# Optimization experiments

Measured on AMD Instinct MI355X. Metric: run time of the kernel, lower is better.

Reference implementation:

```python
import jax, jax.numpy as jnp
import numpy as np
from jax import lax

ALPHA = 2.0   # snntorch surrogate.atan(alpha=2.0)
THR = 1.0     # snntorch Leaky default threshold
NUM_STEPS = 8

@jax.custom_vjp
def spike(x):
    # Heaviside forward, ATan surrogate backward (matches snntorch surrogate.atan)
    return (x > 0).astype(x.dtype)

def _spk_fwd(x):
    return (x > 0).astype(x.dtype), x

def _spk_bwd(x, g):
    return (g * (ALPHA / 2.0) / (1.0 + (jnp.pi / 2.0 * ALPHA * x) ** 2),)

spike.defvjp(_spk_fwd, _spk_bwd)


def setup_inputs() -> dict:
    key = jax.random.key(0)
    ks = jax.random.split(key, 7)
    B, D, H, A = 16384, 512, 2048, 8
    H2 = H // 2
    s1 = 1.0 / np.sqrt(D)
    s2 = 1.0 / np.sqrt(H)
    s3 = 1.0 / np.sqrt(H2)
    return {
        "x": jax.random.normal(ks[0], (B, D), jnp.float32),
        "W1": jax.random.uniform(ks[1], (H, D), jnp.float32, -s1, s1),
        "b1": jax.random.uniform(ks[2], (H,), jnp.float32, -s1, s1),
        "W2": jax.random.uniform(ks[3], (H2, H), jnp.float32, -s2, s2),
        "b2": jax.random.uniform(ks[4], (H2,), jnp.float32, -s2, s2),
        "Wo": jax.random.uniform(ks[5], (A, H2), jnp.float32, -s3, s3),
        "bo": jax.random.uniform(ks[6], (A,), jnp.float32, -s3, s3),
        "beta1": jnp.float32(0.9),
        "beta2": jnp.float32(0.85),
        "beta_out": jnp.float32(0.95),
    }


def reference(x, W1, b1, W2, b2, Wo, bo, beta1, beta2, beta_out):
    B = x.shape[0]
    H, H2, A = W1.shape[0], W2.shape[0], Wo.shape[0]
    # snntorch clamps learnable beta into [0, 1] inside the state function
    be1 = jnp.clip(beta1, 0.0, 1.0)
    be2 = jnp.clip(beta2, 0.0, 1.0)
    beo = jnp.clip(beta_out, 0.0, 1.0)

    cur1 = x @ W1.T + b1  # fc1(x) is identical every step; hoist out of the loop

    mem1 = jnp.zeros((B, H), x.dtype)
    mem2 = jnp.zeros((B, H2), x.dtype)
    mem_out = jnp.zeros((B, A), x.dtype)
    max_mem = jnp.full((B, A), -1e9, x.dtype)

    def step(carry, _):
        mem1, mem2, mem_out, max_mem = carry
        # lif1: subtract-reset Leaky; reset uses detached spike of previous mem
        reset1 = lax.stop_gradient(spike(mem1 - THR))
        mem1 = be1 * mem1 + cur1 - reset1 * THR
        spk1 = spike(mem1 - THR)
        # lif2
        reset2 = lax.stop_gradient(spike(mem2 - THR))
        mem2 = be2 * mem2 + (spk1 @ W2.T + b2) - reset2 * THR
        spk2 = spike(mem2 - THR)
        # li_out: reset_mechanism='none' -> pure leaky integrator
        mem_out = beo * mem_out + (spk2 @ Wo.T + bo)
        max_mem = jnp.maximum(max_mem, mem_out)
        return (mem1, mem2, mem_out, max_mem), None

    (mem1, mem2, mem_out, max_mem), _ = lax.scan(
        step, (mem1, mem2, mem_out, max_mem), None, length=NUM_STEPS
    )
    return max_mem
```

## Files before the change

kernel.cpp:

```cpp
#include <hip/hip_runtime.h>
#include <stdint.h>


typedef __bf16 bf16;
typedef __attribute__((ext_vector_type(8))) __bf16 bf16x8;
typedef __attribute__((ext_vector_type(4))) float f32x4;

#define CAP1 2097152
#define CAP2 2097152
#define MARGIN 2e-3f
#define MARGIN2 5e-4f

__device__ __forceinline__ void gl16(const void* g, void* l) {
  __builtin_amdgcn_global_load_lds(
      (const __attribute__((address_space(1))) uint32_t*)g,
      (__attribute__((address_space(3))) uint32_t*)l, 16, 0, 0);
}

__device__ __forceinline__ float clampf(float v) {
  return fminf(fmaxf(v, 0.f), 1.f);
}

__device__ __forceinline__ uint32_t expand2(uint32_t b) {
  return ((b & 1u) ? 0x3F80u : 0u) | ((b & 2u) ? 0x3F800000u : 0u);
}


__global__ void split_x_kernel(const float* __restrict__ x, bf16* __restrict__ Ax) {
  int i = blockIdx.x * 256 + threadIdx.x;
  int b = i >> 9, d = i & 511;
  float v = x[i];
  bf16 hi = (bf16)v;
  bf16 lo = (bf16)(v - (float)hi);
  size_t base = (size_t)b * 1024;
  Ax[base + d] = hi;
  Ax[base + 512 + d] = lo;
}

__global__ void split_w1_kernel(const float* __restrict__ W1, bf16* __restrict__ B0,
                                bf16* __restrict__ B1) {
  int i = blockIdx.x * 256 + threadIdx.x;
  int r = i >> 9, d = i & 511;
  float v = W1[i];
  bf16 hi = (bf16)v;
  bf16 lo = (bf16)(v - (float)hi);
  size_t base = (size_t)r * 1024;
  B0[base + d] = hi;  B0[base + 512 + d] = lo;
  B1[base + d] = lo;  B1[base + 512 + d] = hi;
}

__global__ void split_w2_kernel(const float* __restrict__ W2, bf16* __restrict__ Wh,
                                bf16* __restrict__ Wl) {
  int i = blockIdx.x * 256 + threadIdx.x;
  float v = W2[i];
  bf16 hi = (bf16)v;
  Wh[i] = hi;
  Wl[i] = (bf16)(v - (float)hi);
}


#define SA_OFF  0
#define SB0_OFF 16384
#define SB1_OFF 32768

__global__ __launch_bounds__(256, 2) void gemm1_lif1_kernel(
    const bf16* __restrict__ A, const bf16* __restrict__ B0,
    const bf16* __restrict__ B1, const float* __restrict__ bias,
    const float* __restrict__ beta1p,
    uint32_t* __restrict__ spkbits1, uint2* __restrict__ flag1,
    uint32_t* __restrict__ cnt1)
{
  __shared__ __align__(16) uint8_t lds[49152];
  const int tid = threadIdx.x;
  const int lane = tid & 63;
  const int wave = tid >> 6;
  const int wm = (wave >> 1) * 64, wn = (wave & 1) * 64;
  const size_t brow = (size_t)blockIdx.x * 128;
  const size_t bcol = (size_t)blockIdx.y * 128;
  const int K = 1024;
  const float be = clampf(beta1p[0]);

  const bf16* gA  = A  + brow * K;
  const bf16* gB0 = B0 + bcol * K;
  const bf16* gB1 = B1 + bcol * K;

  f32x4 acc[4][4] = {};

  for (int kk = 0; kk < K; kk += 64) {
#pragma unroll
    for (int q = 0; q < 4; ++q) {
      const int flat = q * 256 + tid;
      const int row = flat >> 3;
      const int s   = flat & 7;
      const int c8  = (s ^ (row & 7)) * 8;
      gl16(gA  + (size_t)row * K + kk + c8, lds + SA_OFF  + flat * 16);
      gl16(gB0 + (size_t)row * K + kk + c8, lds + SB0_OFF + flat * 16);
      gl16(gB1 + (size_t)row * K + kk + c8, lds + SB1_OFF + flat * 16);
    }
    asm volatile("s_waitcnt vmcnt(0)" ::: "memory");
    __syncthreads();
#pragma unroll
    for (int ks = 0; ks < 2; ++ks) {
      bf16x8 af[4], b0f[4], b1f[4];
#pragma unroll
      for (int i = 0; i < 4; ++i) {
        const int ra = wm + i * 16 + (lane & 15);
        const int sa = ((ks * 4 + (lane >> 4)) ^ (ra & 7)) * 16;
        af[i]  = *(const bf16x8*)(lds + SA_OFF  + ra * 128 + sa);
        const int rb = wn + i * 16 + (lane & 15);
        const int sb = ((ks * 4 + (lane >> 4)) ^ (rb & 7)) * 16;
        b0f[i] = *(const bf16x8*)(lds + SB0_OFF + rb * 128 + sb);
        b1f[i] = *(const bf16x8*)(lds + SB1_OFF + rb * 128 + sb);
      }
#pragma unroll
      for (int m = 0; m < 4; ++m)
#pragma unroll
        for (int n = 0; n < 4; ++n) {
          acc[m][n] = __builtin_amdgcn_mfma_f32_16x16x32_bf16(af[m], b0f[n], acc[m][n], 0, 0, 0);
          acc[m][n] = __builtin_amdgcn_mfma_f32_16x16x32_bf16(af[m], b1f[n], acc[m][n], 0, 0, 0);
        }
    }
    __syncthreads();
  }

  uint32_t* lcnt  = (uint32_t*)lds;
  uint32_t* lbase = (uint32_t*)(lds + 4);
  uint2*    llist = (uint2*)(lds + 16);
  const uint32_t CAPL = 3000;
  if (tid == 0) *lcnt = 0;
  __syncthreads();

  const int rg = lane >> 4;
  const bool writer = (lane & 15) == 0;
  uint16_t* sp16 = (uint16_t*)spkbits1;

#pragma unroll
  for (int m = 0; m < 4; ++m)
#pragma unroll
    for (int n = 0; n < 4; ++n) {
      const int chb = (int)(bcol) + wn + n * 16;
      const int w32 = chb >> 5, half = (chb >> 4) & 1;
      const float bv = bias[chb + (lane & 15)];
#pragma unroll
      for (int j = 0; j < 4; ++j) {
        const float c = acc[m][n][j] + bv;
        float mem = 0.f; uint32_t hist = 0; bool nearThr = false;
#pragma unroll
        for (int t = 0; t < 8; ++t) {
          float rst = (mem > 1.f) ? 1.f : 0.f;
          mem = be * mem + c - rst;
          uint32_t bit = (mem > 1.f) ? 1u : 0u;
          hist |= bit << t;
          nearThr |= (fabsf(mem - 1.f) < MARGIN);
        }
#pragma unroll
        for (int t = 0; t < 8; ++t) {
          unsigned long long bal = __ballot((hist >> t) & 1u);
          if (writer) {
            uint32_t row = (uint32_t)(brow + wm + m * 16 + rg * 4 + j);
            size_t idx = ((size_t)(t * 64 + w32) * 16384 + row) * 2 + half;
            sp16[idx] = (uint16_t)(bal >> (rg * 16));
          }
        }
        if (nearThr) {
          const uint32_t h = (uint32_t)(chb + (lane & 15));
          const uint32_t b = (uint32_t)(brow + wm + m * 16 + rg * 4 + j);
          uint2 en; en.x = (h << 14) | b; en.y = hist;
          uint32_t pos = atomicAdd(lcnt, 1u);
          if (pos < CAPL) llist[pos] = en;
          else { uint32_t g = atomicAdd(cnt1, 1u); if (g < CAP1) flag1[g] = en; }
        }
      }
    }

  __syncthreads();
  uint32_t ln = *lcnt; if (ln > CAPL) ln = CAPL;
  if (tid == 0) *lbase = atomicAdd(cnt1, ln);
  __syncthreads();
  const uint32_t gb = *lbase;
  for (uint32_t i = tid; i < ln; i += 256) {
    uint32_t g = gb + i;
    if (g < CAP1) flag1[g] = llist[i];
  }
}


__global__ __launch_bounds__(256) void repair1_kernel(
    const float* __restrict__ x, const float* __restrict__ W1,
    const float* __restrict__ b1, const float* __restrict__ beta1p,
    const uint2* __restrict__ flag1, const uint32_t* __restrict__ cnt1,
    uint32_t* __restrict__ spkbits1)
{
  uint32_t n = cnt1[0]; if (n > CAP1) n = CAP1;
  const float be = clampf(beta1p[0]);
  for (uint32_t i = blockIdx.x * 256 + threadIdx.x; i < n; i += gridDim.x * 256) {
    uint2 e = flag1[i];
    int h = e.x >> 14, b = e.x & 16383;
    const float* xr = x + (size_t)b * 512;
    const float* wr = W1 + (size_t)h * 512;
    float s = 0.f;
    for (int d = 0; d < 512; ++d) s = fmaf(xr[d], wr[d], s);
    s = __fadd_rn(s, b1[h]);
    float m = 0.f; uint32_t eb = 0;
#pragma unroll
    for (int t = 0; t < 8; ++t) {
      float rst = (__fsub_rn(m, 1.f) > 0.f) ? 1.f : 0.f;
      m = __fsub_rn(__fadd_rn(__fmul_rn(be, m), s), rst);
      if (__fsub_rn(m, 1.f) > 0.f) eb |= 1u << t;
    }
    uint32_t diff = eb ^ (e.y & 0xFFu);
    if (diff) {
#pragma unroll
      for (int t = 0; t < 8; ++t)
        if ((diff >> t) & 1u)
          atomicXor(&spkbits1[((size_t)t * 64 + (h >> 5)) * 16384 + b], 1u << (h & 31));
    }
  }
}


#define BOFF(d) ((d) * 16384)

__global__ __launch_bounds__(256, 3) void step2_kernel(
    const uint32_t* __restrict__ spkbits1,
    const bf16* __restrict__ W2h, const bf16* __restrict__ W2l,
    const float* __restrict__ b2, const float* __restrict__ beta2p,
    uint32_t* __restrict__ spkbits2, uint32_t* __restrict__ flag2,
    uint32_t* __restrict__ cnt2)
{
  __shared__ __align__(16) uint8_t lds[32768];
  const int K = 2048;
  const int tid = threadIdx.x;
  const int lane = tid & 63;
  const int wave = tid >> 6;
  const int wm = (wave >> 1) * 64, wn = (wave & 1) * 64;
  const size_t brow = (size_t)blockIdx.x * 128;
  const size_t bcol = (size_t)blockIdx.y * 128;
  const float be2 = clampf(beta2p[0]);

  const bf16* gB0 = W2h + bcol * K;
  const bf16* gB1 = W2l + bcol * K;

  float b2c[4];
#pragma unroll
  for (int n = 0; n < 4; ++n) b2c[n] = b2[bcol + wn + n * 16 + (lane & 15)];

  const int rg = lane >> 4;
  const int lnlo = lane & 15;
  const int sh8 = rg * 8;
  const bool writer = lnlo == 0;
  uint16_t* sp16 = (uint16_t*)spkbits2;

  f32x4 acc[4][4] = {};
  unsigned long long flg = 0;

#define STAGE_B(D, KC)                                                        \
  {                                                                           \
    _Pragma("unroll")                                                         \
    for (int q = 0; q < 2; ++q) {                                             \
      const int flat = q * 256 + tid;                                         \
      const int row = flat >> 2;                                              \
      const int s = flat & 3;                                                 \
      const int c8 = (s ^ ((row >> 1) & 3)) * 8;                              \
      gl16(gB0 + (size_t)row * K + (KC) * 32 + c8, lds + BOFF(D) + flat * 16);\
      gl16(gB1 + (size_t)row * K + (KC) * 32 + c8,                            \
           lds + BOFF(D) + 8192 + flat * 16);                                 \
    }                                                                         \
  }

#define LOAD_A(AW, TT, KC)                                                    \
  {                                                                           \
    const uint32_t* pA =                                                      \
        spkbits1 + ((size_t)((TT) * 64 + (KC))) * 16384 + brow;               \
    _Pragma("unroll")                                                         \
    for (int i = 0; i < 4; ++i) AW[i] = pA[wm + i * 16 + lnlo];               \
  }

#define CHUNK(CUR, NXT, TT_N, KC_N, D)                                        \
  {                                                                           \
    LOAD_A(NXT, TT_N, KC_N);                                                  \
    STAGE_B(D ^ 1, KC_N);                                                     \
    bf16x8 af[4];                                                             \
    _Pragma("unroll")                                                         \
    for (int i = 0; i < 4; ++i) {                                             \
      uint32_t byte = (CUR[i] >> sh8) & 0xFFu;                                \
      uint4 u;                                                                \
      u.x = expand2(byte);                                                    \
      u.y = expand2(byte >> 2);                                               \
      u.z = expand2(byte >> 4);                                               \
      u.w = expand2(byte >> 6);                                               \
      af[i] = *(bf16x8*)&u;                                                   \
    }                                                                         \
    asm volatile("s_waitcnt vmcnt(8)" ::: "memory");                          \
    __builtin_amdgcn_s_barrier();                                             \
    bf16x8 b0f[4], b1f[4];                                                    \
    _Pragma("unroll")                                                         \
    for (int i = 0; i < 4; ++i) {                                             \
      const int rb = wn + i * 16 + lnlo;                                      \
      const int sb = (rg ^ ((rb >> 1) & 3)) * 16;                             \
      b0f[i] = *(const bf16x8*)(lds + BOFF(D) + rb * 64 + sb);                \
      b1f[i] = *(const bf16x8*)(lds + BOFF(D) + 8192 + rb * 64 + sb);         \
    }                                                                         \
    _Pragma("unroll")                                                         \
    for (int m = 0; m < 4; ++m)                                               \
      _Pragma("unroll")                                                       \
      for (int n = 0; n < 4; ++n) {                                           \
        acc[m][n] = __builtin_amdgcn_mfma_f32_16x16x32_bf16(                  \
            af[m], b0f[n], acc[m][n], 0, 0, 0);                               \
        acc[m][n] = __builtin_amdgcn_mfma_f32_16x16x32_bf16(                  \
            af[m], b1f[n], acc[m][n], 0, 0, 0);                               \
      }                                                                       \
    __builtin_amdgcn_s_barrier();                                             \
  }

  uint32_t awA[4], awB[4];

  LOAD_A(awA, 0, 0);
  STAGE_B(0, 0);

  for (int t = 0; t < 8; ++t) {
#pragma unroll
    for (int m = 0; m < 4; ++m)
#pragma unroll
      for (int n = 0; n < 4; ++n)
#pragma unroll
        for (int j = 0; j < 4; ++j) {
          float v = acc[m][n][j];
          float rst = (v > 1.f) ? 1.f : 0.f;
          acc[m][n][j] = be2 * v + (b2c[n] - rst);
        }

#pragma unroll 1
    for (int kc2 = 0; kc2 < 32; ++kc2) {
      CHUNK(awA, awB, t, 2 * kc2 + 1, 0)
      {
        const int kcn = (2 * kc2 + 2) & 63;
        const int tn = (kc2 == 31 && t < 7) ? t + 1 : t;
        CHUNK(awB, awA, tn, kcn, 1)
      }
    }

#pragma unroll
    for (int m = 0; m < 4; ++m)
#pragma unroll
      for (int n = 0; n < 4; ++n) {
        const int chb = (int)(bcol) + wn + n * 16;
        const int w32 = chb >> 5, half = (chb >> 4) & 1;
#pragma unroll
        for (int j = 0; j < 4; ++j) {
          float v = acc[m][n][j];
          if (fabsf(v - 1.f) < MARGIN2) flg |= 1ull << (m * 16 + n * 4 + j);
          unsigned long long bal = __ballot(v > 1.f);
          if (writer) {
            uint32_t row = (uint32_t)(brow + wm + m * 16 + rg * 4 + j);
            size_t idx = ((size_t)(t * 32 + w32) * 16384 + row) * 2 + half;
            sp16[idx] = (uint16_t)(bal >> (rg * 16));
          }
        }
      }
  }

  asm volatile("s_waitcnt vmcnt(0)" ::: "memory");
  __syncthreads();
  uint32_t* lcnt  = (uint32_t*)lds;
  uint32_t* lbase = (uint32_t*)(lds + 4);
  uint32_t* llist = (uint32_t*)(lds + 16);
  const uint32_t CAPL = 6000;
  if (tid == 0) *lcnt = 0;
  __syncthreads();

  if (flg) {
#pragma unroll
    for (int m = 0; m < 4; ++m)
#pragma unroll
      for (int n = 0; n < 4; ++n)
#pragma unroll
        for (int j = 0; j < 4; ++j)
          if ((flg >> (m * 16 + n * 4 + j)) & 1ull) {
            const int row = wm + m * 16 + rg * 4 + j;
            const int col = wn + n * 16 + lnlo;
            uint32_t en = (uint32_t)(((brow + row) << 10) | (bcol + col));
            uint32_t pos = atomicAdd(lcnt, 1u);
            if (pos < CAPL) llist[pos] = en;
            else { uint32_t g = atomicAdd(cnt2, 1u); if (g < CAP2) flag2[g] = en; }
          }
  }

  __syncthreads();
  uint32_t ln = *lcnt; if (ln > CAPL) ln = CAPL;
  if (tid == 0) *lbase = atomicAdd(cnt2, ln);
  __syncthreads();
  const uint32_t gb = *lbase;
  for (uint32_t i = tid; i < ln; i += 256) {
    uint32_t g = gb + i;
    if (g < CAP2) flag2[g] = llist[i];
  }
#undef STAGE_B
#undef LOAD_A
#undef CHUNK
}


__global__ __launch_bounds__(256) void repair2_kernel(
    const uint32_t* __restrict__ spkbits1, const float* __restrict__ W2,
    const float* __restrict__ b2, const float* __restrict__ beta2p,
    const uint32_t* __restrict__ flag2, const uint32_t* __restrict__ cnt2,
    uint32_t* __restrict__ spkbits2)
{
  uint32_t n = cnt2[0]; if (n > CAP2) n = CAP2;
  const float be = clampf(beta2p[0]);
  for (uint32_t i = blockIdx.x * 256 + threadIdx.x; i < n; i += gridDim.x * 256) {
    uint32_t e = flag2[i];
    int b = e >> 10, h2 = e & 1023;
    const float* wr = W2 + (size_t)h2 * 2048;
    const float bias = b2[h2];
    float s[8] = {0, 0, 0, 0, 0, 0, 0, 0};
    for (int w = 0; w < 64; ++w) {
      uint32_t bt[8];
#pragma unroll
      for (int t = 0; t < 8; ++t)
        bt[t] = spkbits1[((size_t)t * 64 + w) * 16384 + b];
#pragma unroll 8
      for (int k = 0; k < 32; ++k) {
        const float wv = wr[w * 32 + k];
#pragma unroll
        for (int t = 0; t < 8; ++t) {
          float addend = ((bt[t] >> k) & 1u) ? wv : 0.0f;
          s[t] = __fadd_rn(s[t], addend);
        }
      }
    }
    float m = 0.f;
#pragma unroll
    for (int t = 0; t < 8; ++t) {
      float st = __fadd_rn(s[t], bias);
      float rst = (__fsub_rn(m, 1.f) > 0.f) ? 1.f : 0.f;
      m = __fsub_rn(__fadd_rn(__fmul_rn(be, m), st), rst);
      uint32_t exact = (__fsub_rn(m, 1.f) > 0.f) ? 1u : 0u;
      uint32_t* wp = &spkbits2[((size_t)t * 32 + (h2 >> 5)) * 16384 + b];
      uint32_t stored = (*wp >> (h2 & 31)) & 1u;
      if (stored != exact) atomicXor(wp, 1u << (h2 & 31));
    }
  }
}


__global__ __launch_bounds__(256) void out_kernel(
    const uint32_t* __restrict__ spkbits2, const float* __restrict__ Wo,
    const float* __restrict__ bo, const float* __restrict__ betaop,
    float* __restrict__ out)
{
  const int wave = threadIdx.x >> 6, lane = threadIdx.x & 63;
  const int b = blockIdx.x * 4 + wave;
  const float beo = clampf(betaop[0]);
  const int a = lane & 7;
  const int slice = lane >> 3;

  float s[8] = {0, 0, 0, 0, 0, 0, 0, 0};
#pragma unroll
  for (int q = 0; q < 4; ++q) {
    const int wrd = slice * 4 + q;
    uint32_t wt[8];
#pragma unroll
    for (int t = 0; t < 8; ++t)
      wt[t] = spkbits2[((size_t)(t * 32 + wrd)) * 16384 + b];
    const float* wop = Wo + (size_t)a * 1024 + wrd * 32;
#pragma unroll
    for (int k8 = 0; k8 < 8; ++k8) {
      const float4 wv = *(const float4*)(wop + k8 * 4);
      const float wa[4] = {wv.x, wv.y, wv.z, wv.w};
#pragma unroll
      for (int kk = 0; kk < 4; ++kk) {
        const int k = k8 * 4 + kk;
#pragma unroll
        for (int t = 0; t < 8; ++t)
          s[t] += ((wt[t] >> k) & 1u) ? wa[kk] : 0.0f;
      }
    }
  }
#pragma unroll
  for (int t = 0; t < 8; ++t) {
    s[t] += __shfl_down(s[t], 8, 64);
    s[t] += __shfl_down(s[t], 16, 64);
    s[t] += __shfl_down(s[t], 32, 64);
  }
  if (lane < 8) {
    const float bov = bo[a];
    float mo = 0.f, mx = -1e30f;
#pragma unroll
    for (int t = 0; t < 8; ++t) {
      mo = beo * mo + (s[t] + bov);
      mx = fmaxf(mx, mo);
    }
    out[(size_t)b * 8 + a] = mx;
  }
}

__global__ void zero_hdr_kernel(uint32_t* p) {
  if (threadIdx.x < 64) p[threadIdx.x] = 0;
}

__global__ void fill_sentinel(float* out, int n, float v) {
  int i = blockIdx.x * 256 + threadIdx.x;
  if (i < n) out[i] = v;
}


extern "C" void kernel_launch(void* const* d_in, const int* in_sizes, int n_in,
                              void* d_out, int out_size, void* d_ws, size_t ws_size,
                              hipStream_t stream)
{
  (void)in_sizes; (void)n_in;
  const float* x   = (const float*)d_in[0];
  const float* W1  = (const float*)d_in[1];
  const float* b1  = (const float*)d_in[2];
  const float* W2  = (const float*)d_in[3];
  const float* b2  = (const float*)d_in[4];
  const float* Wo  = (const float*)d_in[5];
  const float* bo  = (const float*)d_in[6];
  const float* be1 = (const float*)d_in[7];
  const float* be2 = (const float*)d_in[8];
  const float* beo = (const float*)d_in[9];
  float* out = (float*)d_out;

  const int B = 16384, D = 512, H = 2048, H2 = 1024;

  const size_t sz_hdr  = 256;
  const size_t sz_Ax   = (size_t)B * 1024 * 2;
  const size_t sz_W1s  = (size_t)H * 1024 * 2;
  const size_t sz_W2s  = (size_t)H2 * H * 2;
  const size_t sz_b1   = (size_t)8 * 64 * B * 4;
  const size_t sz_b2   = (size_t)8 * 32 * B * 4;
  const size_t sz_f1   = (size_t)CAP1 * 8;
  const size_t sz_f2   = (size_t)CAP2 * 4;
  const size_t need = sz_hdr + sz_Ax + 2 * sz_W1s + 2 * sz_W2s +
                      sz_b1 + sz_b2 + sz_f1 + sz_f2;

  if (ws_size < need) {
    fill_sentinel<<<(out_size + 255) / 256, 256, 0, stream>>>(
        out, out_size, 1000.0f + (float)(ws_size >> 20));
    return;
  }

  uint8_t* p = (uint8_t*)d_ws;
  uint32_t* hdr = (uint32_t*)p;     p += sz_hdr;
  bf16* Ax      = (bf16*)p;         p += sz_Ax;
  bf16* W1B0    = (bf16*)p;         p += sz_W1s;
  bf16* W1B1    = (bf16*)p;         p += sz_W1s;
  bf16* W2h     = (bf16*)p;         p += sz_W2s;
  bf16* W2l     = (bf16*)p;         p += sz_W2s;
  uint32_t* spkbits1 = (uint32_t*)p; p += sz_b1;
  uint32_t* spkbits2 = (uint32_t*)p; p += sz_b2;
  uint2* flag1  = (uint2*)p;        p += sz_f1;
  uint32_t* flag2 = (uint32_t*)p;   p += sz_f2;
  uint32_t* cnt1 = hdr + 0;
  uint32_t* cnt2 = hdr + 1;

  zero_hdr_kernel<<<1, 64, 0, stream>>>(hdr);
  split_x_kernel <<<(B * D) / 256, 256, 0, stream>>>(x, Ax);
  split_w1_kernel<<<(H * D) / 256, 256, 0, stream>>>(W1, W1B0, W1B1);
  split_w2_kernel<<<(H2 * H) / 256, 256, 0, stream>>>(W2, W2h, W2l);

  gemm1_lif1_kernel<<<dim3(B / 128, H / 128), 256, 0, stream>>>(
      Ax, W1B0, W1B1, b1, be1, spkbits1, flag1, cnt1);
  repair1_kernel<<<256, 256, 0, stream>>>(x, W1, b1, be1, flag1, cnt1, spkbits1);

  step2_kernel<<<dim3(B / 128, H2 / 128), 256, 0, stream>>>(
      spkbits1, W2h, W2l, b2, be2, spkbits2, flag2, cnt2);
  repair2_kernel<<<256, 256, 0, stream>>>(spkbits1, W2, b2, be2, flag2, cnt2, spkbits2);

  out_kernel<<<B / 4, 256, 0, stream>>>(spkbits2, Wo, bo, beo, out);
}
```

Baseline: 2.027 ms.

## Give each wave private LDS staging of W2 tiles and drop block barriers

```diff
diff --git a/kernel.cpp b/kernel.cpp
--- a/kernel.cpp
+++ b/kernel.cpp
@@ -219,16 +219,14 @@
 }
 
 
-#define BOFF(d) ((d) * 16384)
-
-__global__ __launch_bounds__(256, 3) void step2_kernel(
+__global__ __launch_bounds__(256, 2) void step2_kernel(
     const uint32_t* __restrict__ spkbits1,
     const bf16* __restrict__ W2h, const bf16* __restrict__ W2l,
     const float* __restrict__ b2, const float* __restrict__ beta2p,
     uint32_t* __restrict__ spkbits2, uint32_t* __restrict__ flag2,
     uint32_t* __restrict__ cnt2)
 {
-  __shared__ __align__(16) uint8_t lds[32768];
+  __shared__ __align__(16) uint8_t lds[65536];
   const int K = 2048;
   const int tid = threadIdx.x;
   const int lane = tid & 63;
@@ -240,6 +238,7 @@
 
   const bf16* gB0 = W2h + bcol * K;
   const bf16* gB1 = W2l + bcol * K;
+  uint8_t* wlds = lds + wave * 16384;
 
   float b2c[4];
 #pragma unroll
@@ -254,17 +253,17 @@
   f32x4 acc[4][4] = {};
   unsigned long long flg = 0;
 
-#define STAGE_B(D, KC)                                                        \
+#define STAGE_W(D, KC)                                                        \
   {                                                                           \
     _Pragma("unroll")                                                         \
-    for (int q = 0; q < 2; ++q) {                                             \
-      const int flat = q * 256 + tid;                                         \
-      const int row = flat >> 2;                                              \
-      const int s = flat & 3;                                                 \
-      const int c8 = (s ^ ((row >> 1) & 3)) * 8;                              \
-      gl16(gB0 + (size_t)row * K + (KC) * 32 + c8, lds + BOFF(D) + flat * 16);\
-      gl16(gB1 + (size_t)row * K + (KC) * 32 + c8,                            \
-           lds + BOFF(D) + 8192 + flat * 16);                                 \
+    for (int q = 0; q < 4; ++q) {                                             \
+      const int rl = q * 16 + (lane >> 2);                                    \
+      const int s = lane & 3;                                                 \
+      const int c8 = (s ^ ((rl >> 1) & 3)) * 8;                               \
+      gl16(gB0 + (size_t)(wn + rl) * K + (KC) * 32 + c8,                      \
+           wlds + (D) * 8192 + q * 1024 + lane * 16);                         \
+      gl16(gB1 + (size_t)(wn + rl) * K + (KC) * 32 + c8,                      \
+           wlds + (D) * 8192 + 4096 + q * 1024 + lane * 16);                  \
     }                                                                         \
   }
 
@@ -279,7 +278,7 @@
 #define CHUNK(CUR, NXT, TT_N, KC_N, D)                                        \
   {                                                                           \
     LOAD_A(NXT, TT_N, KC_N);                                                  \
-    STAGE_B(D ^ 1, KC_N);                                                     \
+    STAGE_W((D) ^ 1, KC_N);                                                   \
     bf16x8 af[4];                                                             \
     _Pragma("unroll")                                                         \
     for (int i = 0; i < 4; ++i) {                                             \
@@ -291,15 +290,15 @@
       u.w = expand2(byte >> 6);                                               \
       af[i] = *(bf16x8*)&u;                                                   \
     }                                                                         \
-    asm volatile("s_waitcnt vmcnt(8)" ::: "memory");                          \
-    __builtin_amdgcn_s_barrier();                                             \
+    asm volatile("s_waitcnt vmcnt(12)" ::: "memory");                         \
+    __builtin_amdgcn_s_setprio(1);                                            \
     bf16x8 b0f[4], b1f[4];                                                    \
     _Pragma("unroll")                                                         \
     for (int i = 0; i < 4; ++i) {                                             \
-      const int rb = wn + i * 16 + lnlo;                                      \
-      const int sb = (rg ^ ((rb >> 1) & 3)) * 16;                             \
-      b0f[i] = *(const bf16x8*)(lds + BOFF(D) + rb * 64 + sb);                \
-      b1f[i] = *(const bf16x8*)(lds + BOFF(D) + 8192 + rb * 64 + sb);         \
+      const int rbl = i * 16 + lnlo;                                          \
+      const int sb = (rg ^ ((rbl >> 1) & 3)) * 16;                            \
+      b0f[i] = *(const bf16x8*)(wlds + (D) * 8192 + rbl * 64 + sb);           \
+      b1f[i] = *(const bf16x8*)(wlds + (D) * 8192 + 4096 + rbl * 64 + sb);    \
     }                                                                         \
     _Pragma("unroll")                                                         \
     for (int m = 0; m < 4; ++m)                                               \
@@ -310,13 +309,13 @@
         acc[m][n] = __builtin_amdgcn_mfma_f32_16x16x32_bf16(                  \
             af[m], b1f[n], acc[m][n], 0, 0, 0);                               \
       }                                                                       \
-    __builtin_amdgcn_s_barrier();                                             \
+    __builtin_amdgcn_s_setprio(0);                                            \
   }
 
   uint32_t awA[4], awB[4];
 
   LOAD_A(awA, 0, 0);
-  STAGE_B(0, 0);
+  STAGE_W(0, 0);
 
   for (int t = 0; t < 8; ++t) {
 #pragma unroll
@@ -395,7 +394,7 @@
     uint32_t g = gb + i;
     if (g < CAP2) flag2[g] = llist[i];
   }
-#undef STAGE_B
+#undef STAGE_W
 #undef LOAD_A
 #undef CHUNK
 }
```

Measured after the change: 1.954 ms. 3.6% less time.
